# Optimization experiments

Hardware: AMD Instinct MI355X
Metric: run time of the kernel (lower is better)

The kernel has to match this reference:

```python
import jax, jax.numpy as jnp
import numpy as np

N, E = 10000, 160000
RNA, PROT, EMB, HID, H = 2000, 100, 128, 128, 4
D_IN = 2 * EMB          # 256, input to last block
D_MID = HID * 4         # 512, after conv1/lin1 residual (heads*channel)


def _gat(x, src, dst, Ws, Wd, att_s, att_d, bias, n_nodes, heads):
    # PyG GATConv (tuple in_channels -> separate src/dst linears, concat=True,
    # add_self_loops=False, negative_slope=0.2, eval mode so dropout is identity)
    C = Ws.shape[1] // heads
    xs = (x @ Ws).reshape(n_nodes, heads, C)   # [N,H,C]
    xd = (x @ Wd).reshape(n_nodes, heads, C)
    a_s = jnp.sum(xs * att_s, axis=-1)          # [N,H]
    a_d = jnp.sum(xd * att_d, axis=-1)
    alpha = jax.nn.leaky_relu(a_s[src] + a_d[dst], 0.2)   # [E,H]
    m = jax.ops.segment_max(alpha, dst, num_segments=n_nodes)  # [N,H]
    alpha = jnp.exp(alpha - m[dst])
    denom = jax.ops.segment_sum(alpha, dst, num_segments=n_nodes)
    alpha = alpha / (denom[dst] + 1e-16)
    out = jax.ops.segment_sum(xs[src] * alpha[:, :, None], dst, num_segments=n_nodes)
    return out.reshape(n_nodes, heads * C) + bias


def _layernorm(h, g, b, eps=1e-5):
    mu = jnp.mean(h, axis=-1, keepdims=True)
    var = jnp.mean(jnp.square(h - mu), axis=-1, keepdims=True)
    return (h - mu) * jax.lax.rsqrt(var + eps) * g + b


def setup_inputs() -> dict:
    key = jax.random.key(0)
    ks = iter(jax.random.split(key, 40))
    w = lambda *s: jax.random.normal(next(ks), s, jnp.float32) * 0.02
    z = lambda *s: jnp.zeros(s, jnp.float32)
    inp = {}
    inp["x"] = jax.random.normal(next(ks), (N, RNA + PROT), jnp.float32)
    inp["edge_index"] = jax.random.randint(next(ks), (2, E), 0, N, jnp.int64)
    inp["W_rna"], inp["b_rna"] = w(RNA, EMB), z(EMB)
    inp["W_prot"], inp["b_prot"] = w(PROT, EMB), z(EMB)
    # last GraphAttnBlock (hidden_dim -> hidden_dim), the only one whose output is used
    inp["c1_Ws"], inp["c1_Wd"] = w(D_IN, H * HID), w(D_IN, H * HID)
    inp["c1_as"], inp["c1_ad"] = w(H, HID), w(H, HID)
    inp["c1_b"] = z(H * HID)
    inp["l1_W"], inp["l1_b"] = w(D_IN, D_MID), z(D_MID)
    inp["ln_g"], inp["ln_b"] = jnp.ones((D_MID,), jnp.float32), z(D_MID)
    inp["c2_Ws"], inp["c2_Wd"] = w(D_MID, H * HID), w(D_MID, H * HID)
    inp["c2_as"], inp["c2_ad"] = w(H, HID), w(H, HID)
    inp["c2_b"] = z(H * HID)
    inp["l2_W"], inp["l2_b"] = w(D_MID, D_MID), z(D_MID)
    inp["agg_W"], inp["agg_b"] = w(D_MID, HID), z(HID)
    inp["dr_W"], inp["dr_b"] = w(HID, EMB), z(EMB)
    inp["dp_W"], inp["dp_b"] = w(HID, EMB), z(EMB)
    inp["rr_W"], inp["rr_b"] = w(EMB, RNA), z(RNA)
    inp["rp_W"], inp["rp_b"] = w(EMB, PROT), z(PROT)
    return inp


def reference(x, edge_index, W_rna, b_rna, W_prot, b_prot,
              c1_Ws, c1_Wd, c1_as, c1_ad, c1_b, l1_W, l1_b, ln_g, ln_b,
              c2_Ws, c2_Wd, c2_as, c2_ad, c2_b, l2_W, l2_b,
              agg_W, agg_b, dr_W, dr_b, dp_W, dp_b, rr_W, rr_b, rp_W, rp_b):
    src, dst = edge_index[0], edge_index[1]
    rna_e = x[:, :RNA] @ W_rna + b_rna
    prot_e = x[:, RNA:] @ W_prot + b_prot
    xin = jnp.concatenate([rna_e, prot_e], axis=1)   # raw_x_input [N, 2*EMB]
    # source loops blocks over raw_x_input; only last block output survives
    h = _gat(xin, src, dst, c1_Ws, c1_Wd, c1_as, c1_ad, c1_b, N, H) + (xin @ l1_W + l1_b)
    h = jax.nn.relu(_layernorm(h, ln_g, ln_b))
    h = _gat(h, src, dst, c2_Ws, c2_Wd, c2_as, c2_ad, c2_b, N, H) + (h @ l2_W + l2_b)
    emb = jax.nn.relu(h @ agg_W + agg_b)
    rna_recon = (emb @ dr_W + dr_b) @ rr_W + rr_b
    prot_recon = (emb @ dp_W + dp_b) @ rp_W + rp_b
    return (rna_recon, prot_recon, emb)
```

## Files before the change

kernel.cpp:

```cpp
#include <hip/hip_runtime.h>
#include <hip/hip_bf16.h>
#include <stdint.h>
#include <stddef.h>

using bf16  = __hip_bfloat16;
using bf162 = __hip_bfloat162;

typedef __bf16 bvec8 __attribute__((ext_vector_type(8)));
typedef float  fvec4 __attribute__((ext_vector_type(4)));

struct __align__(16) bf16x8 { bf162 a, b, c, d; };

__device__ __forceinline__ void bf8_to_f(const bf16* p, float* o) {
    bf16x8 v = *reinterpret_cast<const bf16x8*>(p);
    o[0] = __bfloat162float(v.a.x); o[1] = __bfloat162float(v.a.y);
    o[2] = __bfloat162float(v.b.x); o[3] = __bfloat162float(v.b.y);
    o[4] = __bfloat162float(v.c.x); o[5] = __bfloat162float(v.c.y);
    o[6] = __bfloat162float(v.d.x); o[7] = __bfloat162float(v.d.y);
}

__device__ __forceinline__ float wred_sum(float v) {
    #pragma unroll
    for (int o = 32; o > 0; o >>= 1) v += __shfl_xor(v, o);
    return v;
}

__device__ __forceinline__ float wred_max(float v) {
    #pragma unroll
    for (int o = 32; o > 0; o >>= 1) v = fmaxf(v, __shfl_xor(v, o));
    return v;
}

__device__ __forceinline__ float lrelu(float x) { return (x > 0.f) ? x : 0.2f * x; }

__device__ __forceinline__ fvec4 mfma16(bvec8 a, bvec8 b, fvec4 c) {
    return __builtin_amdgcn_mfma_f32_16x16x32_bf16(a, b, c, 0, 0, 0);
}

__device__ __forceinline__ bvec8 ldA(const bf16* p) {
    return *reinterpret_cast<const bvec8*>(p);
}
__device__ __forceinline__ bvec8 ldA(const float* p) {
    float4 f0 = *reinterpret_cast<const float4*>(p);
    float4 f1 = *reinterpret_cast<const float4*>(p + 4);
    union { bvec8 v; bf16 h[8]; } u;
    u.h[0] = __float2bfloat16(f0.x); u.h[1] = __float2bfloat16(f0.y);
    u.h[2] = __float2bfloat16(f0.z); u.h[3] = __float2bfloat16(f0.w);
    u.h[4] = __float2bfloat16(f1.x); u.h[5] = __float2bfloat16(f1.y);
    u.h[6] = __float2bfloat16(f1.z); u.h[7] = __float2bfloat16(f1.w);
    return u.v;
}
__device__ __forceinline__ bvec8 ldA_mask(const float* p, int kabs) {
    union { bvec8 v; bf16 h[8]; } u;
    #pragma unroll
    for (int j = 0; j < 8; ++j) {
        float f = (kabs + j < 2100) ? p[j] : 0.f;
        u.h[j] = __float2bfloat16(f);
    }
    return u.v;
}

__global__ void detect_kernel(const int* __restrict__ ei, int E, int* __restrict__ flags) {
    __shared__ int zc;
    if (threadIdx.x == 0) zc = 0;
    __syncthreads();
    int nodd = E / 2; if (nodd > 1024) nodd = 1024;
    for (int i = threadIdx.x; i < nodd; i += blockDim.x)
        if (ei[2 * i + 1] == 0) atomicAdd(&zc, 1);
    __syncthreads();
    if (threadIdx.x == 0) flags[0] = (zc > nodd / 2) ? 1 : 0;
}

__global__ void conv_edges_kernel(const int* __restrict__ ei, int* __restrict__ src32,
                                  int* __restrict__ dst32, int E, int N,
                                  const int* __restrict__ flags) {
    const int e = blockIdx.x * blockDim.x + threadIdx.x;
    if (e >= E) return;
    int s, d;
    if (flags[0]) { s = ei[2 * e]; d = ei[2 * (E + e)]; }
    else          { s = ei[e];     d = ei[E + e]; }
    src32[e] = (s < 0) ? 0 : ((s >= N) ? N - 1 : s);
    dst32[e] = (d < 0) ? 0 : ((d >= N) ? N - 1 : d);
}

__global__ void zero2_kernel(int* __restrict__ p1, int* __restrict__ p2, int n) {
    int i = blockIdx.x * blockDim.x + threadIdx.x;
    if (i < n) { p1[i] = 0; p2[i] = 0; }
}

__global__ void hist_kernel(const int* __restrict__ dst32, int* __restrict__ cnt, int E) {
    int e = blockIdx.x * blockDim.x + threadIdx.x;
    if (e < E) atomicAdd(&cnt[dst32[e]], 1);
}

__global__ void scan_kernel(const int* __restrict__ cnt, int* __restrict__ row_ptr, int N) {
    __shared__ int sh[256];
    __shared__ int carry;
    if (threadIdx.x == 0) { carry = 0; row_ptr[0] = 0; }
    __syncthreads();
    for (int base = 0; base < N; base += 256) {
        int i = base + threadIdx.x;
        int v = (i < N) ? cnt[i] : 0;
        sh[threadIdx.x] = v;
        __syncthreads();
        #pragma unroll
        for (int o = 1; o < 256; o <<= 1) {
            int t = (threadIdx.x >= o) ? sh[threadIdx.x - o] : 0;
            __syncthreads();
            sh[threadIdx.x] += t;
            __syncthreads();
        }
        if (i < N) row_ptr[i + 1] = sh[threadIdx.x] + carry;
        __syncthreads();
        if (threadIdx.x == 0) carry += sh[255];
        __syncthreads();
    }
}

__global__ void fill_csr_kernel(const int* __restrict__ src32, const int* __restrict__ dst32,
                                const int* __restrict__ row_ptr, int* __restrict__ cursor,
                                int* __restrict__ col_src, int E) {
    int e = blockIdx.x * blockDim.x + threadIdx.x;
    if (e >= E) return;
    int d = dst32[e];
    int pos = atomicAdd(&cursor[d], 1);
    col_src[row_ptr[d] + pos] = src32[e];
}

struct WEnt { const float* src; bf16* dst; int K, N, Kp, Np, start; };
struct WTab { WEnt e[12]; int n; };

__global__ __launch_bounds__(256) void wconv_all_kernel(WTab tab) {
    const int b = blockIdx.x;
    int wi = 0;
    #pragma unroll 1
    for (int i = 1; i < tab.n; ++i) if (b >= tab.e[i].start) wi = i;
    const WEnt w = tab.e[wi];
    const int t = (b - w.start) * 256 + threadIdx.x;
    if (t >= w.Np * w.Kp) return;
    const int n = t / w.Kp, k = t - n * w.Kp;
    float v = (n < w.N && k < w.K) ? w.src[(size_t)k * w.N + n] : 0.f;
    w.dst[t] = __float2bfloat16(v);
}

__global__ __launch_bounds__(256) void conv_embB_kernel(const float* __restrict__ Wr,
                                                        const float* __restrict__ Wp,
                                                        bf16* __restrict__ Bt) {
    int t = blockIdx.x * 256 + threadIdx.x;
    if (t >= 256 * 2112) return;
    int n = t / 2112, k = t - n * 2112;
    float v = 0.f;
    if (n < 128) { if (k < 2000) v = Wr[(size_t)k * 128 + n]; }
    else         { if (k >= 2000 && k < 2100) v = Wp[(size_t)(k - 2000) * 128 + (n - 128)]; }
    Bt[t] = __float2bfloat16(v);
}

__global__ void bias_fuse_kernel(const float* l1_b, const float* c1_b, float* bsum1,
                                 const float* l2_b, const float* c2_b, float* bsum2,
                                 const float* dr_b, const float* dp_b, float* ddb,
                                 const float* b_rna, const float* b_prot, float* ebias) {
    int i = blockIdx.x * blockDim.x + threadIdx.x;
    if (i < 512)       bsum1[i] = l1_b[i] + c1_b[i];
    else if (i < 1024) bsum2[i - 512] = l2_b[i - 512] + c2_b[i - 512];
    else if (i < 1152) ddb[i - 1024] = dr_b[i - 1024];
    else if (i < 1280) ddb[i - 1024] = dp_b[i - 1152];
    else if (i < 1408) ebias[i - 1280] = b_rna[i - 1280];
    else if (i < 1536) ebias[i - 1280] = b_prot[i - 1408];
}

__global__ __launch_bounds__(256) void embed_gemm_kernel(
    const float* __restrict__ x, const bf16* __restrict__ Bt,
    float* __restrict__ part, int M)
{
    const int tid = threadIdx.x;
    const int w = tid >> 6, lane = tid & 63;
    const int wr = w >> 1, wc = w & 1;
    const int m0 = blockIdx.y * 64 + wr * 32;
    const int n0 = blockIdx.x * 64 + wc * 32;
    const int z  = blockIdx.z;
    const int lrow = lane & 15;
    const int lk8  = (lane >> 4) * 8;
    const int zp1 = z + 1;
    const int bs = 32 * (z * 16 + (z < 2 ? z : 2));
    const int es = 32 * (zp1 * 16 + (zp1 < 2 ? zp1 : 2));

    int r0 = m0 + lrow;      if (r0 > M - 1) r0 = M - 1;
    int r1 = m0 + 16 + lrow; if (r1 > M - 1) r1 = M - 1;
    const float* Ap0 = x + (size_t)r0 * 2100 + lk8;
    const float* Ap1 = x + (size_t)r1 * 2100 + lk8;
    const bf16*  Bp  = Bt + (size_t)(n0 + lrow) * 2112 + lk8;

    const fvec4 zz = {0.f, 0.f, 0.f, 0.f};
    fvec4 acc00 = zz, acc01 = zz, acc10 = zz, acc11 = zz;

    for (int k = bs; k < es; k += 32) {
        bvec8 b0 = *reinterpret_cast<const bvec8*>(Bp + k);
        bvec8 b1 = *reinterpret_cast<const bvec8*>(Bp + k + 16 * 2112);
        bvec8 a0, a1;
        if (k == 2080) {
            a0 = ldA_mask(Ap0 + k, k + lk8);
            a1 = ldA_mask(Ap1 + k, k + lk8);
        } else {
            a0 = ldA(Ap0 + k);
            a1 = ldA(Ap1 + k);
        }
        acc00 = mfma16(a0, b0, acc00);
        acc10 = mfma16(a1, b0, acc10);
        acc01 = mfma16(a0, b1, acc01);
        acc11 = mfma16(a1, b1, acc11);
    }

    float* pz = part + (size_t)z * M * 256;
    const int r4 = (lane >> 4) * 4;
    #pragma unroll
    for (int fn = 0; fn < 2; ++fn) {
        const int col = n0 + fn * 16 + lrow;
        const fvec4 va = fn ? acc01 : acc00;
        const fvec4 vb = fn ? acc11 : acc10;
        #pragma unroll
        for (int r = 0; r < 4; ++r) {
            int row0 = m0 + r4 + r;
            if (row0 < M) pz[(size_t)row0 * 256 + col] = va[r];
            int row1 = m0 + 16 + r4 + r;
            if (row1 < M) pz[(size_t)row1 * 256 + col] = vb[r];
        }
    }
}

__global__ __launch_bounds__(64) void embed_reduce_logits_kernel(
    const float* __restrict__ part, const float* __restrict__ ebias,
    const float* __restrict__ Vs, const float* __restrict__ Vd,
    bf16* __restrict__ xin_bf, float* __restrict__ a_s, float* __restrict__ a_d, int M)
{
    const int n = blockIdx.x, lane = threadIdx.x;
    const int c0 = lane * 4;
    const size_t base = (size_t)n * 256 + c0;
    float4 v = *reinterpret_cast<const float4*>(part + base);
    #pragma unroll
    for (int z = 1; z < 4; ++z) {
        float4 p = *reinterpret_cast<const float4*>(part + (size_t)z * M * 256 + base);
        v.x += p.x; v.y += p.y; v.z += p.z; v.w += p.w;
    }
    float4 eb = *reinterpret_cast<const float4*>(ebias + c0);
    v.x += eb.x; v.y += eb.y; v.z += eb.z; v.w += eb.w;

    union { bf16 h[4]; uint2 u; } ob;
    ob.h[0] = __float2bfloat16(v.x); ob.h[1] = __float2bfloat16(v.y);
    ob.h[2] = __float2bfloat16(v.z); ob.h[3] = __float2bfloat16(v.w);
    *reinterpret_cast<uint2*>(xin_bf + base) = ob.u;

    const float vv[4] = {v.x, v.y, v.z, v.w};
    float ss0=0,ss1=0,ss2=0,ss3=0, dd0=0,dd1=0,dd2=0,dd3=0;
    #pragma unroll
    for (int j = 0; j < 4; ++j) {
        float4 vs = *reinterpret_cast<const float4*>(Vs + (size_t)(c0 + j) * 4);
        float4 vd = *reinterpret_cast<const float4*>(Vd + (size_t)(c0 + j) * 4);
        ss0 = fmaf(vv[j], vs.x, ss0); ss1 = fmaf(vv[j], vs.y, ss1);
        ss2 = fmaf(vv[j], vs.z, ss2); ss3 = fmaf(vv[j], vs.w, ss3);
        dd0 = fmaf(vv[j], vd.x, dd0); dd1 = fmaf(vv[j], vd.y, dd1);
        dd2 = fmaf(vv[j], vd.z, dd2); dd3 = fmaf(vv[j], vd.w, dd3);
    }
    ss0 = wred_sum(ss0); ss1 = wred_sum(ss1); ss2 = wred_sum(ss2); ss3 = wred_sum(ss3);
    dd0 = wred_sum(dd0); dd1 = wred_sum(dd1); dd2 = wred_sum(dd2); dd3 = wred_sum(dd3);
    if (lane == 0) {
        a_s[n*4+0]=ss0; a_s[n*4+1]=ss1; a_s[n*4+2]=ss2; a_s[n*4+3]=ss3;
        a_d[n*4+0]=dd0; a_d[n*4+1]=dd1; a_d[n*4+2]=dd2; a_d[n*4+3]=dd3;
    }
}

template <int FM, bool RELU, typename AT>
__global__ __launch_bounds__(256) void mfma_gemm_kernel(
    const AT* __restrict__ A, int lda,
    const bf16* __restrict__ Bt, int ldb,
    const float* __restrict__ bias,
    float* __restrict__ Cf, int ldcf,
    bf16* __restrict__ Cb, int ldcb,
    int M, int Nn, int K)
{
    const int tid  = threadIdx.x;
    const int w    = tid >> 6, lane = tid & 63;
    const int wr   = w >> 1,   wc   = w & 1;
    const int m0   = blockIdx.y * (FM * 32) + wr * (FM * 16);
    const int n0   = blockIdx.x * 64 + wc * 32;
    const int lrow = lane & 15;
    const int lk8  = (lane >> 4) * 8;

    const AT* Ap[FM];
    #pragma unroll
    for (int i = 0; i < FM; ++i) {
        int r = m0 + i * 16 + lrow;
        if (r > M - 1) r = M - 1;
        Ap[i] = A + (size_t)r * lda + lk8;
    }
    const bf16* Bp = Bt + (size_t)(n0 + lrow) * ldb + lk8;
    const size_t b16 = (size_t)16 * ldb;

    fvec4 acc[FM][2];
    const fvec4 z = {0.f, 0.f, 0.f, 0.f};
    #pragma unroll
    for (int i = 0; i < FM; ++i) { acc[i][0] = z; acc[i][1] = z; }

    #pragma unroll 2
    for (int k = 0; k < K; k += 32) {
        bvec8 b0 = *reinterpret_cast<const bvec8*>(Bp + k);
        bvec8 b1 = *reinterpret_cast<const bvec8*>(Bp + k + b16);
        #pragma unroll
        for (int i = 0; i < FM; ++i) {
            bvec8 a = ldA(Ap[i] + k);
            acc[i][0] = mfma16(a, b0, acc[i][0]);
            acc[i][1] = mfma16(a, b1, acc[i][1]);
        }
    }

    const int r4 = (lane >> 4) * 4;
    #pragma unroll
    for (int fn = 0; fn < 2; ++fn) {
        const int col = n0 + fn * 16 + lrow;
        if (col >= Nn) continue;
        const float bz = bias ? bias[col] : 0.f;
        #pragma unroll
        for (int fm = 0; fm < FM; ++fm) {
            const int rbase = m0 + fm * 16 + r4;
            #pragma unroll
            for (int r = 0; r < 4; ++r) {
                const int row = rbase + r;
                if (row >= M) continue;
                float v = acc[fm][fn][r] + bz;
                if (RELU) v = fmaxf(v, 0.f);
                if (Cf) Cf[(size_t)row * ldcf + col] = v;
                if (Cb) Cb[(size_t)row * ldcb + col] = __float2bfloat16(v);
            }
        }
    }
}

__global__ __launch_bounds__(256) void mfma_gemm_dual_kernel(
    const bf16* __restrict__ A, int lda,
    const bf16* __restrict__ Bt, int ldb,
    const float* __restrict__ biasU,
    bf16* __restrict__ xs, float* __restrict__ hB,
    int M, int K)
{
    const int tid  = threadIdx.x;
    const int w    = tid >> 6, lane = tid & 63;
    const int wr   = w >> 1,   wc   = w & 1;
    const int m0   = blockIdx.y * 128 + wr * 64;
    const int n0   = blockIdx.x * 64 + wc * 32;
    const int lrow = lane & 15;
    const int lk8  = (lane >> 4) * 8;

    const bf16* Ap[4];
    #pragma unroll
    for (int i = 0; i < 4; ++i) {
        int r = m0 + i * 16 + lrow;
        if (r > M - 1) r = M - 1;
        Ap[i] = A + (size_t)r * lda + lk8;
    }
    const bf16* Bp = Bt + (size_t)(n0 + lrow) * ldb + lk8;
    const size_t b16 = (size_t)16 * ldb;

    fvec4 acc[4][2];
    const fvec4 z = {0.f, 0.f, 0.f, 0.f};
    #pragma unroll
    for (int i = 0; i < 4; ++i) { acc[i][0] = z; acc[i][1] = z; }

    #pragma unroll 2
    for (int k = 0; k < K; k += 32) {
        bvec8 b0 = *reinterpret_cast<const bvec8*>(Bp + k);
        bvec8 b1 = *reinterpret_cast<const bvec8*>(Bp + k + b16);
        #pragma unroll
        for (int i = 0; i < 4; ++i) {
            bvec8 a = *reinterpret_cast<const bvec8*>(Ap[i] + k);
            acc[i][0] = mfma16(a, b0, acc[i][0]);
            acc[i][1] = mfma16(a, b1, acc[i][1]);
        }
    }

    const int r4 = (lane >> 4) * 4;
    #pragma unroll
    for (int fn = 0; fn < 2; ++fn) {
        const int col = n0 + fn * 16 + lrow;
        if (col < 512) {
            #pragma unroll
            for (int fm = 0; fm < 4; ++fm) {
                const int rbase = m0 + fm * 16 + r4;
                #pragma unroll
                for (int r = 0; r < 4; ++r) {
                    const int row = rbase + r;
                    if (row >= M) continue;
                    xs[(size_t)row * 512 + col] = __float2bfloat16(acc[fm][fn][r]);
                }
            }
        } else {
            const int c2 = col - 512;
            const float bz = biasU[c2];
            #pragma unroll
            for (int fm = 0; fm < 4; ++fm) {
                const int rbase = m0 + fm * 16 + r4;
                #pragma unroll
                for (int r = 0; r < 4; ++r) {
                    const int row = rbase + r;
                    if (row >= M) continue;
                    hB[(size_t)row * 512 + c2] = acc[fm][fn][r] + bz;
                }
            }
        }
    }
}

__global__ void make_v2_kernel(const float* __restrict__ Ws, const float* __restrict__ atts,
                               float* __restrict__ Vs,
                               const float* __restrict__ Wd, const float* __restrict__ attd,
                               float* __restrict__ Vd, int K)
{
    int t = blockIdx.x * blockDim.x + threadIdx.x;
    const int half = K * 4;
    if (t >= 2 * half) return;
    const float* W   = (t < half) ? Ws : Wd;
    const float* att = (t < half) ? atts : attd;
    float* V         = (t < half) ? Vs : Vd;
    int tt = (t < half) ? t : t - half;
    int k = tt >> 2, h = tt & 3;
    float s = 0.f;
    const float* wp = W + (size_t)k * 512 + h * 128;
    const float* ap = att + h * 128;
    #pragma unroll 4
    for (int c = 0; c < 128; ++c)
        s = fmaf(wp[c], ap[c], s);
    V[k * 4 + h] = s;
}

__global__ __launch_bounds__(64) void gat_gather_kernel(
    const int* __restrict__ row_ptr, const int* __restrict__ col_src,
    const float* __restrict__ a_s, const float* __restrict__ a_d,
    const bf16* __restrict__ xs, float* __restrict__ hout,
    bf16* __restrict__ hout_bf)
{
    const int d = blockIdx.x, lane = threadIdx.x;
    const int beg = row_ptr[d], end = row_ptr[d + 1];
    const float4 ad = *reinterpret_cast<const float4*>(a_d + (size_t)d * 4);

    float m0=-1e30f, m1=-1e30f, m2=-1e30f, m3=-1e30f;
    for (int i = beg + lane; i < end; i += 64) {
        int s = col_src[i];
        float4 as = *reinterpret_cast<const float4*>(a_s + (size_t)s * 4);
        m0 = fmaxf(m0, lrelu(as.x + ad.x));
        m1 = fmaxf(m1, lrelu(as.y + ad.y));
        m2 = fmaxf(m2, lrelu(as.z + ad.z));
        m3 = fmaxf(m3, lrelu(as.w + ad.w));
    }
    m0 = wred_max(m0); m1 = wred_max(m1); m2 = wred_max(m2); m3 = wred_max(m3);

    float d0=0.f, d1=0.f, d2=0.f, d3=0.f;
    for (int i = beg + lane; i < end; i += 64) {
        int s = col_src[i];
        float4 as = *reinterpret_cast<const float4*>(a_s + (size_t)s * 4);
        d0 += __expf(lrelu(as.x + ad.x) - m0);
        d1 += __expf(lrelu(as.y + ad.y) - m1);
        d2 += __expf(lrelu(as.z + ad.z) - m2);
        d3 += __expf(lrelu(as.w + ad.w) - m3);
    }
    d0 = wred_sum(d0); d1 = wred_sum(d1); d2 = wred_sum(d2); d3 = wred_sum(d3);

    const int h = lane >> 4;
    const float mh   = (h == 0) ? m0 : ((h == 1) ? m1 : ((h == 2) ? m2 : m3));
    const float adh  = (h == 0) ? ad.x : ((h == 1) ? ad.y : ((h == 2) ? ad.z : ad.w));
    const float den  = (h == 0) ? d0 : ((h == 1) ? d1 : ((h == 2) ? d2 : d3));
    const float invd = 1.0f / (den + 1e-16f);
    const int c0 = lane * 8;
    float acc[8] = {0.f,0.f,0.f,0.f,0.f,0.f,0.f,0.f};
    #pragma unroll 2
    for (int i = beg; i < end; ++i) {
        int s = col_src[i];
        float coef = __expf(lrelu(a_s[(size_t)s * 4 + h] + adh) - mh) * invd;
        float xv[8];
        bf8_to_f(xs + (size_t)s * 512 + c0, xv);
        #pragma unroll
        for (int t = 0; t < 8; ++t) acc[t] = fmaf(coef, xv[t], acc[t]);
    }
    float* hp = hout + (size_t)d * 512 + c0;
    if (hout_bf) {
        bf16* hb = hout_bf + (size_t)d * 512 + c0;
        #pragma unroll
        for (int t = 0; t < 8; ++t) {
            float fv = hp[t] + acc[t];
            hp[t] = fv;
            hb[t] = __float2bfloat16(fv);
        }
    } else {
        #pragma unroll
        for (int t = 0; t < 8; ++t) hp[t] += acc[t];
    }
}

__global__ __launch_bounds__(64) void ln_relu_logits_kernel(
    const float* __restrict__ in, const float* __restrict__ g,
    const float* __restrict__ b,
    const float* __restrict__ Vs, const float* __restrict__ Vd,
    bf16* __restrict__ outbf, float* __restrict__ a_s, float* __restrict__ a_d)
{
    const int n = blockIdx.x, lane = threadIdx.x;
    const int c0 = lane * 8;
    const float* ip = in + (size_t)n * 512 + c0;
    float v[8];
    float4 p0 = *reinterpret_cast<const float4*>(ip);
    float4 p1 = *reinterpret_cast<const float4*>(ip + 4);
    v[0]=p0.x; v[1]=p0.y; v[2]=p0.z; v[3]=p0.w; v[4]=p1.x; v[5]=p1.y; v[6]=p1.z; v[7]=p1.w;
    float s = 0.f;
    #pragma unroll
    for (int t = 0; t < 8; ++t) s += v[t];
    s = wred_sum(s);
    const float mu = s * (1.0f / 512.0f);
    float q = 0.f;
    #pragma unroll
    for (int t = 0; t < 8; ++t) { float dlt = v[t] - mu; q = fmaf(dlt, dlt, q); }
    q = wred_sum(q);
    const float sc = rsqrtf(q * (1.0f / 512.0f) + 1e-5f);
    float4 g0 = *reinterpret_cast<const float4*>(g + c0);
    float4 g1 = *reinterpret_cast<const float4*>(g + c0 + 4);
    float4 b0 = *reinterpret_cast<const float4*>(b + c0);
    float4 b1 = *reinterpret_cast<const float4*>(b + c0 + 4);
    const float gv[8] = {g0.x,g0.y,g0.z,g0.w,g1.x,g1.y,g1.z,g1.w};
    const float bv[8] = {b0.x,b0.y,b0.z,b0.w,b1.x,b1.y,b1.z,b1.w};
    float r[8];
    bf16* ob = outbf + (size_t)n * 512 + c0;
    #pragma unroll
    for (int t = 0; t < 8; ++t) {
        r[t] = fmaxf(0.f, fmaf((v[t] - mu) * sc, gv[t], bv[t]));
        ob[t] = __float2bfloat16(r[t]);
    }
    float ss0=0,ss1=0,ss2=0,ss3=0, dd0=0,dd1=0,dd2=0,dd3=0;
    #pragma unroll
    for (int t = 0; t < 8; ++t) {
        float4 vs = *reinterpret_cast<const float4*>(Vs + (size_t)(c0 + t) * 4);
        float4 vd = *reinterpret_cast<const float4*>(Vd + (size_t)(c0 + t) * 4);
        ss0 = fmaf(r[t], vs.x, ss0); ss1 = fmaf(r[t], vs.y, ss1);
        ss2 = fmaf(r[t], vs.z, ss2); ss3 = fmaf(r[t], vs.w, ss3);
        dd0 = fmaf(r[t], vd.x, dd0); dd1 = fmaf(r[t], vd.y, dd1);
        dd2 = fmaf(r[t], vd.z, dd2); dd3 = fmaf(r[t], vd.w, dd3);
    }
    ss0 = wred_sum(ss0); ss1 = wred_sum(ss1); ss2 = wred_sum(ss2); ss3 = wred_sum(ss3);
    dd0 = wred_sum(dd0); dd1 = wred_sum(dd1); dd2 = wred_sum(dd2); dd3 = wred_sum(dd3);
    if (lane == 0) {
        a_s[n*4+0]=ss0; a_s[n*4+1]=ss1; a_s[n*4+2]=ss2; a_s[n*4+3]=ss3;
        a_d[n*4+0]=dd0; a_d[n*4+1]=dd1; a_d[n*4+2]=dd2; a_d[n*4+3]=dd3;
    }
}

extern "C" void kernel_launch(void* const* d_in, const int* in_sizes, int n_in,
                              void* d_out, int out_size, void* d_ws, size_t ws_size,
                              hipStream_t stream)
{
    (void)n_in; (void)out_size; (void)ws_size;
    const float* x   = (const float*)d_in[0];
    const int*   ei  = (const int*)d_in[1];

    const float* W_rna  = (const float*)d_in[2];
    const float* b_rna  = (const float*)d_in[3];
    const float* W_prot = (const float*)d_in[4];
    const float* b_prot = (const float*)d_in[5];
    const float* c1_Ws  = (const float*)d_in[6];
    const float* c1_Wd  = (const float*)d_in[7];
    const float* c1_as  = (const float*)d_in[8];
    const float* c1_ad  = (const float*)d_in[9];
    const float* c1_b   = (const float*)d_in[10];
    const float* l1_W   = (const float*)d_in[11];
    const float* l1_b   = (const float*)d_in[12];
    const float* ln_g   = (const float*)d_in[13];
    const float* ln_b   = (const float*)d_in[14];
    const float* c2_Ws  = (const float*)d_in[15];
    const float* c2_Wd  = (const float*)d_in[16];
    const float* c2_as  = (const float*)d_in[17];
    const float* c2_ad  = (const float*)d_in[18];
    const float* c2_b   = (const float*)d_in[19];
    const float* l2_W   = (const float*)d_in[20];
    const float* l2_b   = (const float*)d_in[21];
    const float* agg_W  = (const float*)d_in[22];
    const float* agg_b  = (const float*)d_in[23];
    const float* dr_W   = (const float*)d_in[24];
    const float* dr_b   = (const float*)d_in[25];
    const float* dp_W   = (const float*)d_in[26];
    const float* dp_b   = (const float*)d_in[27];
    const float* rr_W   = (const float*)d_in[28];
    const float* rr_b   = (const float*)d_in[29];
    const float* rp_W   = (const float*)d_in[30];
    const float* rp_b   = (const float*)d_in[31];

    const int N = in_sizes[0] / 2100;
    const int E = in_sizes[1] / 2;
    const int Mp = ((N + 127) & ~127) + 128;

    char* wsp = (char*)d_ws;
    size_t off = 0;
    auto alloc = [&](size_t bytes) -> void* {
        void* p = wsp + off;
        off += (bytes + 255) & ~(size_t)255;
        return p;
    };
    int*      flags   = (int*)   alloc(16);
    int*      src32   = (int*)   alloc((size_t)E * 4);
    int*      dst32   = (int*)   alloc((size_t)E * 4);
    int*      cnt     = (int*)   alloc((size_t)N * 4);
    int*      cursor  = (int*)   alloc((size_t)N * 4);
    int*      row_ptr = (int*)   alloc((size_t)(N + 1) * 4);
    int*      col_src = (int*)   alloc((size_t)E * 4);
    float*    part    = (float*) alloc((size_t)4 * N * 256 * 4);
    float*    hB      = (float*) alloc((size_t)N * 512 * 4);
    float*    a_s     = (float*) alloc((size_t)N * 4 * 4);
    float*    a_d     = (float*) alloc((size_t)N * 4 * 4);
    float*    Vs      = (float*) alloc(512 * 4 * 4);
    float*    Vd      = (float*) alloc(512 * 4 * 4);
    float*    bsum1   = (float*) alloc(512 * 4);
    float*    bsum2   = (float*) alloc(512 * 4);
    float*    ddb     = (float*) alloc(256 * 4);
    float*    ebias   = (float*) alloc(256 * 4);
    bf16*     xin_bf  = (bf16*)  alloc((size_t)Mp * 256 * 2);
    bf16*     hA_bf   = (bf16*)  alloc((size_t)Mp * 512 * 2);
    bf16*     hB_bf   = (bf16*)  alloc((size_t)Mp * 512 * 2);
    bf16*     xs      = (bf16*)  alloc((size_t)Mp * 512 * 2);
    bf16*     emb_bf  = (bf16*)  alloc((size_t)Mp * 128 * 2);
    bf16*     trp     = (bf16*)  alloc((size_t)Mp * 256 * 2);
    bf16*     embBt   = (bf16*)  alloc((size_t)256 * 2112 * 2);
    bf16*     cb1     = (bf16*)  alloc((size_t)1024 * 256 * 2);
    bf16*     cb2     = (bf16*)  alloc((size_t)1024 * 512 * 2);
    bf16*     aggt    = (bf16*)  alloc((size_t)128 * 512 * 2);
    bf16*     ddt     = (bf16*)  alloc((size_t)256 * 128 * 2);
    bf16*     rrt     = (bf16*)  alloc((size_t)2048 * 128 * 2);
    bf16*     rpt     = (bf16*)  alloc((size_t)128 * 128 * 2);

    const dim3 blk64(64, 1, 1);
    const dim3 blk256(256, 1, 1);
    const dim3 gE((E + 255) / 256);
    const dim3 gN((N + 255) / 256);
    const int GY128 = (N + 127) / 128;
    const int GY64  = (N + 63) / 64;

    float* out0 = (float*)d_out;
    float* out1 = out0 + (size_t)N * 2000;
    float* out2 = out1 + (size_t)N * 100;

    detect_kernel<<<dim3(1), blk256, 0, stream>>>(ei, E, flags);
    conv_edges_kernel<<<gE, blk256, 0, stream>>>(ei, src32, dst32, E, N, flags);
    zero2_kernel<<<gN, blk256, 0, stream>>>(cnt, cursor, N);
    hist_kernel<<<gE, blk256, 0, stream>>>(dst32, cnt, E);
    scan_kernel<<<dim3(1), blk256, 0, stream>>>(cnt, row_ptr, N);
    fill_csr_kernel<<<gE, blk256, 0, stream>>>(src32, dst32, row_ptr, cursor, col_src, E);

    {
        WTab tab{};
        int nb = 0, i = 0;
        auto add = [&](const float* s, bf16* d, int K, int Nn, int Kp, int Np) {
            tab.e[i] = {s, d, K, Nn, Kp, Np, nb};
            nb += (Np * Kp + 255) / 256;
            ++i;
        };
        add(c1_Ws,  cb1,              256, 512,  256, 512);
        add(l1_W,   cb1 + 512 * 256,  256, 512,  256, 512);
        add(c2_Ws,  cb2,              512, 512,  512, 512);
        add(l2_W,   cb2 + 512 * 512,  512, 512,  512, 512);
        add(agg_W,  aggt,             512, 128,  512, 128);
        add(dr_W,   ddt,              128, 128,  128, 128);
        add(dp_W,   ddt + 128 * 128,  128, 128,  128, 128);
        add(rr_W,   rrt,              128, 2000, 128, 2048);
        add(rp_W,   rpt,              128, 100,  128, 128);
        tab.n = i;
        wconv_all_kernel<<<dim3(nb), blk256, 0, stream>>>(tab);
    }
    conv_embB_kernel<<<dim3(256 * 2112 / 256), blk256, 0, stream>>>(W_rna, W_prot, embBt);
    bias_fuse_kernel<<<dim3(6), blk256, 0, stream>>>(l1_b, c1_b, bsum1,
                                                     l2_b, c2_b, bsum2,
                                                     dr_b, dp_b, ddb,
                                                     b_rna, b_prot, ebias);
    make_v2_kernel<<<dim3((2 * 256 * 4 + 255) / 256), blk256, 0, stream>>>(
        c1_Ws, c1_as, Vs, c1_Wd, c1_ad, Vd, 256);

    embed_gemm_kernel<<<dim3(4, GY64, 4), blk256, 0, stream>>>(x, embBt, part, N);
    embed_reduce_logits_kernel<<<dim3(N), blk64, 0, stream>>>(
        part, ebias, Vs, Vd, xin_bf, a_s, a_d, N);

    mfma_gemm_dual_kernel<<<dim3(16, GY128), blk256, 0, stream>>>(
        xin_bf, 256, cb1, 256, bsum1, xs, hB, N, 256);
    gat_gather_kernel<<<dim3(N), blk64, 0, stream>>>(row_ptr, col_src, a_s, a_d, xs, hB, nullptr);

    make_v2_kernel<<<dim3((2 * 512 * 4 + 255) / 256), blk256, 0, stream>>>(
        c2_Ws, c2_as, Vs, c2_Wd, c2_ad, Vd, 512);
    ln_relu_logits_kernel<<<dim3(N), blk64, 0, stream>>>(
        hB, ln_g, ln_b, Vs, Vd, hA_bf, a_s, a_d);

    mfma_gemm_dual_kernel<<<dim3(16, GY128), blk256, 0, stream>>>(
        hA_bf, 512, cb2, 512, bsum2, xs, hB, N, 512);
    gat_gather_kernel<<<dim3(N), blk64, 0, stream>>>(row_ptr, col_src, a_s, a_d, xs, hB, hB_bf);

    mfma_gemm_kernel<2, true, bf16><<<dim3(2, GY64), blk256, 0, stream>>>(
        hB_bf, 512, aggt, 512, agg_b, out2, 128, emb_bf, 128, N, 128, 512);
    mfma_gemm_kernel<2, false, bf16><<<dim3(4, GY64), blk256, 0, stream>>>(
        emb_bf, 128, ddt, 128, ddb, nullptr, 0, trp, 256, N, 256, 128);
    mfma_gemm_kernel<4, false, bf16><<<dim3(32, GY128), blk256, 0, stream>>>(
        trp, 256, rrt, 128, rr_b, out0, 2000, nullptr, 0, N, 2000, 128);
    mfma_gemm_kernel<2, false, bf16><<<dim3(2, GY64), blk256, 0, stream>>>(
        trp + 128, 256, rpt, 128, rp_b, out1, 100, nullptr, 0, N, 100, 128);
}
```

Measured before the change: 681.3 us.

## Replace split-K embed GEMM with full-K row-strip kernel fusing bias and bf16 output

The embedding GEMM drops its 4-way split-K with fp32 partial buffers. Each 1024-thread block now owns a 16-row strip across all 256 output columns and runs the full K loop, adding bias and writing bf16 xin directly. Because the x strip is shared by 16 waves in one block, each x row is read from HBM once, where before it was read by four column blocks. The partial-sum write and reduce pass go away, and the logit computation moves to a small kernel that reads bf16 xin, which slightly changes precision and gives longer per-wave K loops with less parallelism per block.

```diff
diff --git a/kernel.cpp b/kernel.cpp
--- a/kernel.cpp
+++ b/kernel.cpp
@@ -168,88 +168,56 @@
     else if (i < 1536) ebias[i - 1280] = b_prot[i - 1408];
 }
 
-__global__ __launch_bounds__(256) void embed_gemm_kernel(
+__global__ __launch_bounds__(1024) void embed_gemm_kernel(
     const float* __restrict__ x, const bf16* __restrict__ Bt,
-    float* __restrict__ part, int M)
-{
-    const int tid = threadIdx.x;
-    const int w = tid >> 6, lane = tid & 63;
-    const int wr = w >> 1, wc = w & 1;
-    const int m0 = blockIdx.y * 64 + wr * 32;
-    const int n0 = blockIdx.x * 64 + wc * 32;
-    const int z  = blockIdx.z;
+    const float* __restrict__ ebias, bf16* __restrict__ xin_bf, int M)
+{
+    const int tid  = threadIdx.x;
+    const int w    = tid >> 6, lane = tid & 63;
+    const int m0   = blockIdx.x * 16;
+    const int n0   = w * 16;
     const int lrow = lane & 15;
     const int lk8  = (lane >> 4) * 8;
-    const int zp1 = z + 1;
-    const int bs = 32 * (z * 16 + (z < 2 ? z : 2));
-    const int es = 32 * (zp1 * 16 + (zp1 < 2 ? zp1 : 2));
-
-    int r0 = m0 + lrow;      if (r0 > M - 1) r0 = M - 1;
-    int r1 = m0 + 16 + lrow; if (r1 > M - 1) r1 = M - 1;
-    const float* Ap0 = x + (size_t)r0 * 2100 + lk8;
-    const float* Ap1 = x + (size_t)r1 * 2100 + lk8;
-    const bf16*  Bp  = Bt + (size_t)(n0 + lrow) * 2112 + lk8;
-
-    const fvec4 zz = {0.f, 0.f, 0.f, 0.f};
-    fvec4 acc00 = zz, acc01 = zz, acc10 = zz, acc11 = zz;
-
-    for (int k = bs; k < es; k += 32) {
+
+    int r = m0 + lrow; if (r > M - 1) r = M - 1;
+    const float* Ap = x + (size_t)r * 2100 + lk8;
+    const bf16*  Bp = Bt + (size_t)(n0 + lrow) * 2112 + lk8;
+
+    fvec4 acc = {0.f, 0.f, 0.f, 0.f};
+    #pragma unroll 2
+    for (int k = 0; k < 2080; k += 32) {
         bvec8 b0 = *reinterpret_cast<const bvec8*>(Bp + k);
-        bvec8 b1 = *reinterpret_cast<const bvec8*>(Bp + k + 16 * 2112);
-        bvec8 a0, a1;
-        if (k == 2080) {
-            a0 = ldA_mask(Ap0 + k, k + lk8);
-            a1 = ldA_mask(Ap1 + k, k + lk8);
-        } else {
-            a0 = ldA(Ap0 + k);
-            a1 = ldA(Ap1 + k);
-        }
-        acc00 = mfma16(a0, b0, acc00);
-        acc10 = mfma16(a1, b0, acc10);
-        acc01 = mfma16(a0, b1, acc01);
-        acc11 = mfma16(a1, b1, acc11);
-    }
-
-    float* pz = part + (size_t)z * M * 256;
-    const int r4 = (lane >> 4) * 4;
-    #pragma unroll
-    for (int fn = 0; fn < 2; ++fn) {
-        const int col = n0 + fn * 16 + lrow;
-        const fvec4 va = fn ? acc01 : acc00;
-        const fvec4 vb = fn ? acc11 : acc10;
-        #pragma unroll
-        for (int r = 0; r < 4; ++r) {
-            int row0 = m0 + r4 + r;
-            if (row0 < M) pz[(size_t)row0 * 256 + col] = va[r];
-            int row1 = m0 + 16 + r4 + r;
-            if (row1 < M) pz[(size_t)row1 * 256 + col] = vb[r];
-        }
-    }
-}
-
-__global__ __launch_bounds__(64) void embed_reduce_logits_kernel(
-    const float* __restrict__ part, const float* __restrict__ ebias,
+        bvec8 a0 = ldA(Ap + k);
+        acc = mfma16(a0, b0, acc);
+    }
+    {
+        bvec8 b0 = *reinterpret_cast<const bvec8*>(Bp + 2080);
+        bvec8 a0 = ldA_mask(Ap + 2080, 2080 + lk8);
+        acc = mfma16(a0, b0, acc);
+    }
+
+    const int col = n0 + lrow;
+    const int r4  = (lane >> 4) * 4;
+    const float bz = ebias[col];
+    #pragma unroll
+    for (int rr = 0; rr < 4; ++rr) {
+        const int row = m0 + r4 + rr;
+        if (row < M)
+            xin_bf[(size_t)row * 256 + col] = __float2bfloat16(acc[rr] + bz);
+    }
+}
+
+__global__ __launch_bounds__(64) void logits_bf16_kernel(
+    const bf16* __restrict__ X,
     const float* __restrict__ Vs, const float* __restrict__ Vd,
-    bf16* __restrict__ xin_bf, float* __restrict__ a_s, float* __restrict__ a_d, int M)
+    float* __restrict__ a_s, float* __restrict__ a_d)
 {
     const int n = blockIdx.x, lane = threadIdx.x;
     const int c0 = lane * 4;
-    const size_t base = (size_t)n * 256 + c0;
-    float4 v = *reinterpret_cast<const float4*>(part + base);
-    #pragma unroll
-    for (int z = 1; z < 4; ++z) {
-        float4 p = *reinterpret_cast<const float4*>(part + (size_t)z * M * 256 + base);
-        v.x += p.x; v.y += p.y; v.z += p.z; v.w += p.w;
-    }
-    float4 eb = *reinterpret_cast<const float4*>(ebias + c0);
-    v.x += eb.x; v.y += eb.y; v.z += eb.z; v.w += eb.w;
-
-    union { bf16 h[4]; uint2 u; } ob;
-    ob.h[0] = __float2bfloat16(v.x); ob.h[1] = __float2bfloat16(v.y);
-    ob.h[2] = __float2bfloat16(v.z); ob.h[3] = __float2bfloat16(v.w);
-    *reinterpret_cast<uint2*>(xin_bf + base) = ob.u;
-
-    const float vv[4] = {v.x, v.y, v.z, v.w};
+    union { uint2 u; bf16 h[4]; } ub;
+    ub.u = *reinterpret_cast<const uint2*>(X + (size_t)n * 256 + c0);
+    const float vv[4] = {__bfloat162float(ub.h[0]), __bfloat162float(ub.h[1]),
+                         __bfloat162float(ub.h[2]), __bfloat162float(ub.h[3])};
     float ss0=0,ss1=0,ss2=0,ss3=0, dd0=0,dd1=0,dd2=0,dd3=0;
     #pragma unroll
     for (int j = 0; j < 4; ++j) {
@@ -604,7 +572,6 @@
     int*      cursor  = (int*)   alloc((size_t)N * 4);
     int*      row_ptr = (int*)   alloc((size_t)(N + 1) * 4);
     int*      col_src = (int*)   alloc((size_t)E * 4);
-    float*    part    = (float*) alloc((size_t)4 * N * 256 * 4);
     float*    hB      = (float*) alloc((size_t)N * 512 * 4);
     float*    a_s     = (float*) alloc((size_t)N * 4 * 4);
     float*    a_d     = (float*) alloc((size_t)N * 4 * 4);
@@ -674,9 +641,9 @@
     make_v2_kernel<<<dim3((2 * 256 * 4 + 255) / 256), blk256, 0, stream>>>(
         c1_Ws, c1_as, Vs, c1_Wd, c1_ad, Vd, 256);
 
-    embed_gemm_kernel<<<dim3(4, GY64, 4), blk256, 0, stream>>>(x, embBt, part, N);
-    embed_reduce_logits_kernel<<<dim3(N), blk64, 0, stream>>>(
-        part, ebias, Vs, Vd, xin_bf, a_s, a_d, N);
+    embed_gemm_kernel<<<dim3((N + 15) / 16), dim3(1024, 1, 1), 0, stream>>>(
+        x, embBt, ebias, xin_bf, N);
+    logits_bf16_kernel<<<dim3(N), blk64, 0, stream>>>(xin_bf, Vs, Vd, a_s, a_d);
 
     mfma_gemm_dual_kernel<<<dim3(16, GY128), blk256, 0, stream>>>(
         xin_bf, 256, cb1, 256, bsum1, xs, hB, N, 256);
```

Result: slower. 756.8 us (+11.1%).
